# Kernel tuning notes

Hardware: AMD Instinct MI355X
Metric: run time of the kernel (lower is better)

The kernel has to match this reference:

```python
import jax, jax.numpy as jnp
import numpy as np

B, T, I, H = 32, 2048, 256, 512
STD = 0.075


def setup_inputs() -> dict:
    key = jax.random.key(0)
    ks = jax.random.split(key, 7)
    x = jax.random.normal(ks[0], (B, T, I), dtype=jnp.float32)
    # Linear weights: normal(mean=0, std=0.075); biases: PyTorch default uniform(-1/sqrt(fan_in), 1/sqrt(fan_in))
    u_w = STD * jax.random.normal(ks[1], (H, I), dtype=jnp.float32)
    u_b = jax.random.uniform(ks[2], (H,), minval=-1.0 / np.sqrt(I), maxval=1.0 / np.sqrt(I), dtype=jnp.float32)
    w_w = STD * jax.random.normal(ks[3], (H, H), dtype=jnp.float32)
    w_b = jax.random.uniform(ks[4], (H,), minval=-1.0 / np.sqrt(H), maxval=1.0 / np.sqrt(H), dtype=jnp.float32)
    o_w = STD * jax.random.normal(ks[5], (I, H), dtype=jnp.float32)
    o_b = jax.random.uniform(ks[6], (I,), minval=-1.0 / np.sqrt(H), maxval=1.0 / np.sqrt(H), dtype=jnp.float32)
    return {"x": x, "u_w": u_w, "u_b": u_b, "w_w": w_w, "w_b": w_b, "o_w": o_w, "o_b": o_b}


def reference(x, u_w, u_b, w_w, w_b, o_w, o_b):
    # Precompute input projection for all steps at once: [B, T, H]
    xu = jnp.einsum('bti,hi->bth', x, u_w) + u_b

    def step(hidden, xu_t):
        # hidden: [B, H]; xu_t: [B, H]
        hidden = jnp.tanh(xu_t + hidden @ w_w.T + w_b)
        return hidden, hidden

    h0 = jnp.zeros((x.shape[0], w_w.shape[0]), dtype=x.dtype)
    _, hs = jax.lax.scan(step, h0, jnp.swapaxes(xu, 0, 1))  # hs: [T, B, H]
    out = jnp.swapaxes(hs, 0, 1)  # [B, T, H]
    return jax.nn.sigmoid(jnp.einsum('bth,ih->bti', out, o_w) + o_b)
```

## Files before the change

kernel.cpp:

```cpp
#include <hip/hip_runtime.h>
#include <cstdint>
#include <cstddef>

#define B_ 32
#define T_ 2048
#define I_ 256
#define H_ 512
#define G_ 16
#define SLICE (H_/G_)

typedef float  f32x4  __attribute__((ext_vector_type(4)));
typedef __bf16 bf16x8 __attribute__((ext_vector_type(8)));

__device__ __forceinline__ f32x4 MFMA(bf16x8 a, bf16x8 b, f32x4 c) {
    return __builtin_amdgcn_mfma_f32_16x16x32_bf16(a, b, c, 0, 0, 0);
}

__device__ __forceinline__ bf16x8 cvt8v(float4 a, float4 b) {
    bf16x8 r;
    r[0] = (__bf16)a.x; r[1] = (__bf16)a.y; r[2] = (__bf16)a.z; r[3] = (__bf16)a.w;
    r[4] = (__bf16)b.x; r[5] = (__bf16)b.y; r[6] = (__bf16)b.z; r[7] = (__bf16)b.w;
    return r;
}

__device__ __forceinline__ f32x4 xu_step(const float* xp, const bf16x8 uf[8]) {
    float4 xr[16];
#pragma unroll
    for (int kc = 0; kc < 8; ++kc) {
        xr[2*kc]   = *(const float4*)(xp + kc*32);
        xr[2*kc+1] = *(const float4*)(xp + kc*32 + 4);
    }
    f32x4 a = {0.f, 0.f, 0.f, 0.f};
#pragma unroll
    for (int kc = 0; kc < 8; ++kc)
        a = MFMA(cvt8v(xr[2*kc], xr[2*kc+1]), uf[kc], a);
    return a;
}

__global__ __launch_bounds__(512, 1) void rnn_scan(
    const float* __restrict__ x, const float* __restrict__ u_w,
    const float* __restrict__ u_b, const float* __restrict__ w_w,
    const float* __restrict__ w_b, __bf16* __restrict__ hs ,
    __bf16* hbuf , unsigned* bar )
{
    const int tid = threadIdx.x;
    const int wv  = tid >> 6;
    const int ln  = tid & 63;
    const int l15 = ln & 15, lq = ln >> 4;
    const int base = blockIdx.x * SLICE;

    __shared__ f32x4 xup[4][64];

    unsigned* cnt  = bar;
    unsigned* flag = bar + 32;

    if (wv < 4) {
        const int mh = wv >> 1, nh = wv & 1;
        const int ho = base + nh*16 + l15;
        bf16x8 wf[16];
#pragma unroll
        for (int kc = 0; kc < 16; ++kc) {
            const float* p = w_w + (size_t)ho*H_ + kc*32 + lq*8;
            wf[kc] = cvt8v(*(const float4*)p, *(const float4*)(p+4));
        }
        const float bias = u_b[ho] + w_b[ho];
        const int arow  = mh*16 + l15;
        const int crow0 = mh*16 + lq*4;

        for (int t = 0; t < T_; ++t) {
            const __bf16* cur = hbuf + (size_t)(t & 1) * (B_*H_);
            const __bf16* ap  = cur + (size_t)arow*H_ + lq*8;
            f32x4 acc0 = {0.f,0.f,0.f,0.f}, acc1 = {0.f,0.f,0.f,0.f};
#pragma unroll
            for (int kc = 0; kc < 16; kc += 2) {
                bf16x8 a0 = *(const bf16x8*)(ap + kc*32);
                bf16x8 a1 = *(const bf16x8*)(ap + (kc+1)*32);
                acc0 = MFMA(a0, wf[kc],   acc0);
                acc1 = MFMA(a1, wf[kc+1], acc1);
            }
            __syncthreads();
            f32x4 xv = xup[wv][ln];
            __bf16* nxt = hbuf + (size_t)((t+1) & 1) * (B_*H_);
#pragma unroll
            for (int r = 0; r < 4; ++r) {
                float v = acc0[r] + acc1[r] + xv[r] + bias;
                float e = __expf(2.f * v);
                float h = 1.f - 2.f/(e + 1.f);
                __bf16 hb = (__bf16)h;
                const int brow = crow0 + r;
                nxt[(size_t)brow*H_ + ho] = hb;
                hs[((size_t)brow*T_ + t)*H_ + ho] = hb;
            }
            __threadfence();
            __syncthreads();
            if (tid == 0) {
                unsigned old = atomicAdd(cnt, 1u);
                if (old == (unsigned)(G_*(t+1) - 1))
                    __hip_atomic_store(flag, (unsigned)(t+1),
                                       __ATOMIC_RELEASE, __HIP_MEMORY_SCOPE_AGENT);
                else
                    while (__hip_atomic_load(flag, __ATOMIC_ACQUIRE,
                                             __HIP_MEMORY_SCOPE_AGENT) < (unsigned)(t+1)) {}
                __threadfence();
            }
            __syncthreads();
        }
    } else {
        const int wx = wv - 4, mh = wx >> 1, nh = wx & 1;
        const int ho = base + nh*16 + l15;
        bf16x8 uf[8];
#pragma unroll
        for (int kc = 0; kc < 8; ++kc) {
            const float* p = u_w + (size_t)ho*I_ + kc*32 + lq*8;
            uf[kc] = cvt8v(*(const float4*)p, *(const float4*)(p+4));
        }
        const int arow = mh*16 + l15;
        const float* xp0 = x + (size_t)arow*(T_*I_) + lq*8;
        f32x4 acc = xu_step(xp0, uf);
        for (int t = 0; t < T_; ++t) {
            xup[wx][ln] = acc;
            __syncthreads();
            const int tt = (t+1 < T_) ? (t+1) : (T_-1);
            acc = xu_step(xp0 + (size_t)tt*I_, uf);
            __threadfence();
            __syncthreads();
            __syncthreads();
        }
    }
}

__global__ void cvt_ow(const float* __restrict__ ow, __bf16* __restrict__ owb) {
    int i = blockIdx.x * blockDim.x + threadIdx.x;
    if (i < I_*H_) owb[i] = (__bf16)ow[i];
}

__global__ __launch_bounds__(256, 1) void out_proj(
    const __bf16* hs, const __bf16* __restrict__ owb,
    const float* __restrict__ o_b, float* out)
{
    const int tid = threadIdx.x, wv = tid >> 6, ln = tid & 63;
    const int l15 = ln & 15, lq = ln >> 4;
    const size_t m0 = (size_t)blockIdx.x * 32;
    const __bf16* a0p = hs + (m0 + l15)*H_ + lq*8;
    const __bf16* a1p = a0p + (size_t)16*H_;
    f32x4 acc[2][4] = {};
#pragma unroll
    for (int kc = 0; kc < 16; ++kc) {
        bf16x8 a0 = *(const bf16x8*)(a0p + kc*32);
        bf16x8 a1 = *(const bf16x8*)(a1p + kc*32);
#pragma unroll
        for (int nt = 0; nt < 4; ++nt) {
            const __bf16* bp = owb + (size_t)(wv*64 + nt*16 + l15)*H_ + kc*32 + lq*8;
            bf16x8 b = *(const bf16x8*)bp;
            acc[0][nt] = MFMA(a0, b, acc[0][nt]);
            acc[1][nt] = MFMA(a1, b, acc[1][nt]);
        }
    }
    __syncthreads();
#pragma unroll
    for (int nt = 0; nt < 4; ++nt) {
        const int col = wv*64 + nt*16 + l15;
        const float ob = o_b[col];
#pragma unroll
        for (int mt = 0; mt < 2; ++mt) {
#pragma unroll
            for (int r = 0; r < 4; ++r) {
                const size_t row = m0 + mt*16 + lq*4 + r;
                float v = acc[mt][nt][r] + ob;
                out[row*I_ + col] = 1.f/(1.f + __expf(-v));
            }
        }
    }
}

extern "C" void kernel_launch(void* const* d_in, const int* in_sizes, int n_in,
                              void* d_out, int out_size, void* d_ws, size_t ws_size,
                              hipStream_t stream)
{
    const float* x   = (const float*)d_in[0];
    const float* u_w = (const float*)d_in[1];
    const float* u_b = (const float*)d_in[2];
    const float* w_w = (const float*)d_in[3];
    const float* w_b = (const float*)d_in[4];
    const float* o_w = (const float*)d_in[5];
    const float* o_b = (const float*)d_in[6];

    char* ws = (char*)d_ws;
    __bf16*   hbuf = (__bf16*)ws;
    unsigned* bar  = (unsigned*)(ws + 65536);
    __bf16*   owb  = (__bf16*)(ws + 65536 + 256);

    hipMemsetAsync(d_ws, 0, 65536 + 256, stream);
    cvt_ow<<<dim3(512), dim3(256), 0, stream>>>(o_w, owb);
    rnn_scan<<<dim3(G_), dim3(512), 0, stream>>>(x, u_w, u_b, w_w, w_b,
                                                 (__bf16*)d_out, hbuf, bar);
    out_proj<<<dim3((B_*T_)/32), dim3(256), 0, stream>>>((const __bf16*)d_out, owb,
                                                         o_b, (float*)d_out);
}
```

Baseline: 15.19 ms.

## Restructure RNN scan onto two workgroups with per-wave flags and LDS staging

The recurrent scan now runs on 2 workgroups of 8 waves instead of 16 workgroups, and each wave owns 32 hidden columns for all 32 batch rows. The global counter barrier is replaced by per-wave step flags that consumers poll with relaxed atomics. The previous hidden state is staged into swizzled LDS once per step, and the x·U projection is computed inline by the same waves from a pre-converted bf16 U. The aim is to cut cross-workgroup barrier latency and the per-step fan-in. In exchange, each step has fewer compute units doing more serial work, and correctness depends on relaxed-atomic ordering plus an explicit vmcnt wait.

```diff
diff --git a/kernel.cpp b/kernel.cpp
--- a/kernel.cpp
+++ b/kernel.cpp
@@ -6,11 +6,10 @@
 #define T_ 2048
 #define I_ 256
 #define H_ 512
-#define G_ 16
-#define SLICE (H_/G_)
 
 typedef float  f32x4  __attribute__((ext_vector_type(4)));
 typedef __bf16 bf16x8 __attribute__((ext_vector_type(8)));
+typedef unsigned long long u64;
 
 __device__ __forceinline__ f32x4 MFMA(bf16x8 a, bf16x8 b, f32x4 c) {
     return __builtin_amdgcn_mfma_f32_16x16x32_bf16(a, b, c, 0, 0, 0);
@@ -23,115 +22,128 @@
     return r;
 }
 
-__device__ __forceinline__ f32x4 xu_step(const float* xp, const bf16x8 uf[8]) {
-    float4 xr[16];
-#pragma unroll
-    for (int kc = 0; kc < 8; ++kc) {
-        xr[2*kc]   = *(const float4*)(xp + kc*32);
-        xr[2*kc+1] = *(const float4*)(xp + kc*32 + 4);
-    }
-    f32x4 a = {0.f, 0.f, 0.f, 0.f};
-#pragma unroll
-    for (int kc = 0; kc < 8; ++kc)
-        a = MFMA(cvt8v(xr[2*kc], xr[2*kc+1]), uf[kc], a);
-    return a;
-}
-
-__global__ __launch_bounds__(512, 1) void rnn_scan(
-    const float* __restrict__ x, const float* __restrict__ u_w,
+__global__ __launch_bounds__(512) void rnn_scan2(
+    const float* __restrict__ x, const __bf16* __restrict__ uwb,
     const float* __restrict__ u_b, const float* __restrict__ w_w,
     const float* __restrict__ w_b, __bf16* __restrict__ hs ,
-    __bf16* hbuf , unsigned* bar )
+    __bf16* __restrict__ hbuf , unsigned* __restrict__ flags)
 {
-    const int tid = threadIdx.x;
-    const int wv  = tid >> 6;
-    const int ln  = tid & 63;
+    __shared__ char smem[65536];
+    const int tid = threadIdx.x, wv = tid >> 6, ln = tid & 63;
     const int l15 = ln & 15, lq = ln >> 4;
-    const int base = blockIdx.x * SLICE;
-
-    __shared__ f32x4 xup[4][64];
-
-    unsigned* cnt  = bar;
-    unsigned* flag = bar + 32;
-
-    if (wv < 4) {
-        const int mh = wv >> 1, nh = wv & 1;
-        const int ho = base + nh*16 + l15;
-        bf16x8 wf[16];
+    const int wg  = blockIdx.x;
+    const int gwv = wg*8 + wv;
+    const int col0 = wg*256 + wv*32;
+    const int ho0 = col0 + l15, ho1 = ho0 + 16;
+
+    bf16x8 wf[2][16];
+#pragma unroll
+    for (int nt = 0; nt < 2; ++nt) {
+        const float* wp = w_w + (size_t)(nt ? ho1 : ho0)*H_ + lq*8;
+#pragma unroll
+        for (int kc = 0; kc < 16; ++kc)
+            wf[nt][kc] = cvt8v(*(const float4*)(wp + kc*32),
+                               *(const float4*)(wp + kc*32 + 4));
+    }
+    const float bias0 = u_b[ho0] + w_b[ho0];
+    const float bias1 = u_b[ho1] + w_b[ho1];
+
+    f32x4 xacc[2][2];
+    auto xu_compute = [&](int t1) {
+#pragma unroll
+        for (int mt = 0; mt < 2; ++mt)
+#pragma unroll
+            for (int nt = 0; nt < 2; ++nt) xacc[mt][nt] = (f32x4){0.f,0.f,0.f,0.f};
+#pragma unroll
+        for (int kc = 0; kc < 8; ++kc) {
+            const float* xp0 = x + ((size_t)l15*T_ + t1)*I_ + kc*32 + lq*8;
+            const float* xp1 = x + ((size_t)(16 + l15)*T_ + t1)*I_ + kc*32 + lq*8;
+            bf16x8 a0 = cvt8v(*(const float4*)xp0, *(const float4*)(xp0 + 4));
+            bf16x8 a1 = cvt8v(*(const float4*)xp1, *(const float4*)(xp1 + 4));
+            bf16x8 u0 = *(const bf16x8*)(uwb + (size_t)ho0*I_ + kc*32 + lq*8);
+            bf16x8 u1 = *(const bf16x8*)(uwb + (size_t)ho1*I_ + kc*32 + lq*8);
+            xacc[0][0] = MFMA(a0, u0, xacc[0][0]);
+            xacc[0][1] = MFMA(a0, u1, xacc[0][1]);
+            xacc[1][0] = MFMA(a1, u0, xacc[1][0]);
+            xacc[1][1] = MFMA(a1, u1, xacc[1][1]);
+        }
+    };
+    xu_compute(0);
+
+    for (int t = 0; t < T_; ++t) {
+        if (t) {
+            const unsigned* fp = flags + (l15 << 4);
+            for (;;) {
+                unsigned f = __hip_atomic_load(fp, __ATOMIC_RELAXED,
+                                               __HIP_MEMORY_SCOPE_AGENT);
+                if (__all(f >= (unsigned)t)) break;
+            }
+        }
+        const char* curg = (const char*)hbuf + (t & 1)*32768;
+        char* sbase = smem + (t & 1)*32768;
+        {
+            const u64* gsrc = (const u64*)(curg + (wv*4096 + ln*64));
+            u64 q[8];
+#pragma unroll
+            for (int j = 0; j < 8; ++j)
+                q[j] = __hip_atomic_load(gsrc + j, __ATOMIC_RELAXED,
+                                         __HIP_MEMORY_SCOPE_AGENT);
+            const unsigned baseb = (unsigned)(wv*4096 + ln*64);
+            const unsigned swz   = ((baseb >> 10) & 7) << 4;
+#pragma unroll
+            for (int j = 0; j < 4; ++j) {
+                uint4 w4 = make_uint4((unsigned)q[2*j], (unsigned)(q[2*j] >> 32),
+                                      (unsigned)q[2*j+1], (unsigned)(q[2*j+1] >> 32));
+                *(uint4*)(sbase + ((baseb + j*16) ^ swz)) = w4;
+            }
+        }
+        __syncthreads();
+        f32x4 acc[2][2] = {};
+        const unsigned swz0 = (unsigned)((l15 & 7) << 4);
+        const unsigned b0 = (unsigned)(l15*1024 + lq*16);
+        const unsigned b1 = b0 + 16*1024;
 #pragma unroll
         for (int kc = 0; kc < 16; ++kc) {
-            const float* p = w_w + (size_t)ho*H_ + kc*32 + lq*8;
-            wf[kc] = cvt8v(*(const float4*)p, *(const float4*)(p+4));
-        }
-        const float bias = u_b[ho] + w_b[ho];
-        const int arow  = mh*16 + l15;
-        const int crow0 = mh*16 + lq*4;
-
-        for (int t = 0; t < T_; ++t) {
-            const __bf16* cur = hbuf + (size_t)(t & 1) * (B_*H_);
-            const __bf16* ap  = cur + (size_t)arow*H_ + lq*8;
-            f32x4 acc0 = {0.f,0.f,0.f,0.f}, acc1 = {0.f,0.f,0.f,0.f};
-#pragma unroll
-            for (int kc = 0; kc < 16; kc += 2) {
-                bf16x8 a0 = *(const bf16x8*)(ap + kc*32);
-                bf16x8 a1 = *(const bf16x8*)(ap + (kc+1)*32);
-                acc0 = MFMA(a0, wf[kc],   acc0);
-                acc1 = MFMA(a1, wf[kc+1], acc1);
-            }
-            __syncthreads();
-            f32x4 xv = xup[wv][ln];
-            __bf16* nxt = hbuf + (size_t)((t+1) & 1) * (B_*H_);
+            bf16x8 a0 = *(const bf16x8*)(sbase + ((b0 + kc*64) ^ swz0));
+            bf16x8 a1 = *(const bf16x8*)(sbase + ((b1 + kc*64) ^ swz0));
+            acc[0][0] = MFMA(a0, wf[0][kc], acc[0][0]);
+            acc[0][1] = MFMA(a0, wf[1][kc], acc[0][1]);
+            acc[1][0] = MFMA(a1, wf[0][kc], acc[1][0]);
+            acc[1][1] = MFMA(a1, wf[1][kc], acc[1][1]);
+        }
+        __bf16* nxtg = hbuf + ((t + 1) & 1)*(B_*H_);
+#pragma unroll
+        for (int mt = 0; mt < 2; ++mt)
+#pragma unroll
+        for (int nt = 0; nt < 2; ++nt) {
+            const int col = nt ? ho1 : ho0;
+            const float bs = nt ? bias1 : bias0;
 #pragma unroll
             for (int r = 0; r < 4; ++r) {
-                float v = acc0[r] + acc1[r] + xv[r] + bias;
+                float v = acc[mt][nt][r] + xacc[mt][nt][r] + bs;
                 float e = __expf(2.f * v);
                 float h = 1.f - 2.f/(e + 1.f);
                 __bf16 hb = (__bf16)h;
-                const int brow = crow0 + r;
-                nxt[(size_t)brow*H_ + ho] = hb;
-                hs[((size_t)brow*T_ + t)*H_ + ho] = hb;
-            }
-            __threadfence();
-            __syncthreads();
-            if (tid == 0) {
-                unsigned old = atomicAdd(cnt, 1u);
-                if (old == (unsigned)(G_*(t+1) - 1))
-                    __hip_atomic_store(flag, (unsigned)(t+1),
-                                       __ATOMIC_RELEASE, __HIP_MEMORY_SCOPE_AGENT);
-                else
-                    while (__hip_atomic_load(flag, __ATOMIC_ACQUIRE,
-                                             __HIP_MEMORY_SCOPE_AGENT) < (unsigned)(t+1)) {}
-                __threadfence();
-            }
-            __syncthreads();
-        }
-    } else {
-        const int wx = wv - 4, mh = wx >> 1, nh = wx & 1;
-        const int ho = base + nh*16 + l15;
-        bf16x8 uf[8];
-#pragma unroll
-        for (int kc = 0; kc < 8; ++kc) {
-            const float* p = u_w + (size_t)ho*I_ + kc*32 + lq*8;
-            uf[kc] = cvt8v(*(const float4*)p, *(const float4*)(p+4));
-        }
-        const int arow = mh*16 + l15;
-        const float* xp0 = x + (size_t)arow*(T_*I_) + lq*8;
-        f32x4 acc = xu_step(xp0, uf);
-        for (int t = 0; t < T_; ++t) {
-            xup[wx][ln] = acc;
-            __syncthreads();
-            const int tt = (t+1 < T_) ? (t+1) : (T_-1);
-            acc = xu_step(xp0 + (size_t)tt*I_, uf);
-            __threadfence();
-            __syncthreads();
-            __syncthreads();
-        }
-    }
-}
-
-__global__ void cvt_ow(const float* __restrict__ ow, __bf16* __restrict__ owb) {
+                unsigned short us; __builtin_memcpy(&us, &hb, 2);
+                const int brow = mt*16 + lq*4 + r;
+                __hip_atomic_store((unsigned short*)(nxtg + (size_t)brow*H_ + col),
+                                   us, __ATOMIC_RELAXED, __HIP_MEMORY_SCOPE_AGENT);
+                hs[((size_t)brow*T_ + t)*H_ + col] = hb;
+            }
+        }
+        asm volatile("s_waitcnt vmcnt(0)" ::: "memory");
+        if (ln == 0)
+            __hip_atomic_store(flags + (gwv << 4), (unsigned)(t + 1),
+                               __ATOMIC_RELAXED, __HIP_MEMORY_SCOPE_AGENT);
+        if (t + 1 < T_) xu_compute(t + 1);
+    }
+}
+
+__global__ void cvt_wb(const float* __restrict__ uw, const float* __restrict__ ow,
+                       __bf16* __restrict__ uwb, __bf16* __restrict__ owb) {
     int i = blockIdx.x * blockDim.x + threadIdx.x;
-    if (i < I_*H_) owb[i] = (__bf16)ow[i];
+    if (i < H_*I_) uwb[i] = (__bf16)uw[i];
+    else { int j = i - H_*I_; if (j < I_*H_) owb[j] = (__bf16)ow[j]; }
 }
 
 __global__ __launch_bounds__(256, 1) void out_proj(
@@ -186,14 +198,15 @@
     const float* o_b = (const float*)d_in[6];
 
     char* ws = (char*)d_ws;
-    __bf16*   hbuf = (__bf16*)ws;
-    unsigned* bar  = (unsigned*)(ws + 65536);
-    __bf16*   owb  = (__bf16*)(ws + 65536 + 256);
-
-    hipMemsetAsync(d_ws, 0, 65536 + 256, stream);
-    cvt_ow<<<dim3(512), dim3(256), 0, stream>>>(o_w, owb);
-    rnn_scan<<<dim3(G_), dim3(512), 0, stream>>>(x, u_w, u_b, w_w, w_b,
-                                                 (__bf16*)d_out, hbuf, bar);
+    __bf16*   hbuf  = (__bf16*)ws;
+    unsigned* flags = (unsigned*)(ws + 65536);
+    __bf16*   uwb   = (__bf16*)(ws + 131072);
+    __bf16*   owb   = (__bf16*)(ws + 393216);
+
+    hipMemsetAsync(d_ws, 0, 66560, stream);
+    cvt_wb<<<dim3((2*H_*I_)/256), dim3(256), 0, stream>>>(u_w, o_w, uwb, owb);
+    rnn_scan2<<<dim3(2), dim3(512), 0, stream>>>(x, uwb, u_b, w_w, w_b,
+                                                 (__bf16*)d_out, hbuf, flags);
     out_proj<<<dim3((B_*T_)/32), dim3(256), 0, stream>>>((const __bf16*)d_out, owb,
                                                          o_b, (float*)d_out);
 }
```

Measured after the change: 36.58 ms. 2.41x slower.
